# Performance work log

Hardware: AMD Instinct MI355X
Metric: run time of the kernel (lower is better)

## Reference

```python
import jax, jax.numpy as jnp
import numpy as np

PI = float(np.pi)
C64 = jnp.complex64

# ---- gate matrices (PennyLane conventions) ----

def _rx(t):
    c = jnp.cos(t / 2); s = jnp.sin(t / 2)
    return jnp.array([[c, -1j * s], [-1j * s, c]]).astype(C64)

def _rz(t):
    return jnp.array([[jnp.exp(-0.5j * t), 0.0], [0.0, jnp.exp(0.5j * t)]]).astype(C64)

def _rot(phi, th, om):
    # Rot(phi, theta, omega) = RZ(omega) RY(theta) RZ(phi)
    c = jnp.cos(th / 2); s = jnp.sin(th / 2)
    return jnp.array([
        [jnp.exp(-0.5j * (phi + om)) * c, -jnp.exp(0.5j * (phi - om)) * s],
        [jnp.exp(-0.5j * (phi - om)) * s,  jnp.exp(0.5j * (phi + om)) * c],
    ]).astype(C64)

def _crx(t):
    c = jnp.cos(t / 2); s = jnp.sin(t / 2)
    return jnp.array([
        [1, 0, 0, 0],
        [0, 1, 0, 0],
        [0, 0, c, -1j * s],
        [0, 0, -1j * s, c],
    ]).astype(C64)

CNOT = jnp.array([[1, 0, 0, 0], [0, 1, 0, 0], [0, 0, 0, 1], [0, 0, 1, 0]], dtype=C64)

# ---- state-vector primitives (state shape (2,)*n) ----

def _ap1(psi, U, w):
    return jnp.moveaxis(jnp.tensordot(U, psi, axes=((1,), (w,))), 0, w)

def _ap2(psi, U, a, b):
    U = U.reshape(2, 2, 2, 2)
    return jnp.moveaxis(jnp.tensordot(U, psi, axes=((2, 3), (a, b))), (0, 1), (a, b))

def _expZ(psi, w):
    p = jnp.moveaxis(jnp.abs(psi) ** 2, w, 0)
    return (p[0] - p[1]).sum()

def _expX(psi, w):
    return jnp.real(jnp.sum(jnp.conj(psi) * jnp.flip(psi, axis=w)))

# wire pairs in initQKV_on_wires order
_PAIRS = [(0, 1), (1, 2), (2, 3), (3, 0), (0, 3), (1, 0), (2, 1), (3, 2)]

def _init_qkv(psi, rot_p, crx_p, off):
    for i, (a, b) in enumerate(_PAIRS):
        psi = _ap1(psi, _rot(rot_p[3 * i], rot_p[3 * i + 1], rot_p[3 * i + 2]), off + a)
        psi = _ap2(psi, _crx(crx_p[i]), off + a, off + b)
        psi = _ap2(psi, CNOT, off + a, off + b)
    return psi

def _sample(x, qr, qc, kr, kc, vr, vc):
    # qmha_score: 8-qubit circuit
    psi = jnp.zeros((2,) * 8, C64).at[(0,) * 8].set(1.0)
    for w in range(4):  # AngleEmbedding (RX) of xq
        psi = _ap1(psi, _rx(x[w]), w)
    psi = _init_qkv(psi, qr, qc, 0)
    for w in range(4):  # AngleEmbedding (RX) of xk (same x)
        psi = _ap1(psi, _rx(x[w]), w)
    psi = _init_qkv(psi, kr, kc, 4)
    for w in range(4):
        psi = _ap2(psi, CNOT, w, w + 4)
    z = jnp.stack([_expZ(psi, w) for w in range(4)])
    xm = jnp.stack([_expX(psi, w) for w in range(4)])
    score = jnp.sqrt(z * z + xm * xm)
    # qmha_value: 4-qubit circuit
    phi = jnp.zeros((2,) * 4, C64).at[(0,) * 4].set(1.0)
    for w in range(4):
        phi = _ap1(phi, _rx(x[w]), w)
    phi = _init_qkv(phi, vr, vc, 0)
    for w in range(4):
        phi = _ap1(phi, _rz(jnp.tanh(score[w]) * PI), w)
    for a, b in [(0, 1), (1, 2), (2, 3)]:
        phi = _ap2(phi, CNOT, a, b)
    zv = jnp.stack([_expZ(phi, w) for w in range(4)])
    xv = jnp.stack([_expX(phi, w) for w in range(4)])
    return jnp.concatenate([zv, xv])  # [8]


def setup_inputs() -> dict:
    key = jax.random.key(0)
    ks = jax.random.split(key, 12)
    B = 16384
    u = lambda k, n: jax.random.uniform(k, (n,), jnp.float32, -PI / 2, PI / 2)
    return {
        "x1": jax.random.normal(ks[0], (B, 96), jnp.float32),
        "pre_w": jax.random.normal(ks[1], (4, 96), jnp.float32) / np.sqrt(96.0),
        "pre_b": jnp.zeros((4,), jnp.float32),
        "q_rot": u(ks[2], 24),
        "k_rot": u(ks[3], 24),
        "v_rot": u(ks[4], 24),
        "q_crx": 0.1 * jax.random.normal(ks[5], (8,), jnp.float32),
        "k_crx": 0.1 * jax.random.normal(ks[6], (8,), jnp.float32),
        "v_crx": 0.1 * jax.random.normal(ks[7], (8,), jnp.float32),
        "ln_w": jnp.ones((8,), jnp.float32),
        "ln_b": jnp.zeros((8,), jnp.float32),
        "head_w": jax.random.normal(ks[8], (2, 8), jnp.float32) / np.sqrt(8.0),
        "head_b": jnp.zeros((2,), jnp.float32),
    }


def reference(x1, pre_w, pre_b, q_rot, k_rot, v_rot, q_crx, k_crx, v_crx,
              ln_w, ln_b, head_w, head_b):
    x = x1 @ pre_w.T + pre_b  # [B, 4] angles
    outs = jax.vmap(lambda xi: _sample(xi, q_rot, q_crx, k_rot, k_crx, v_rot, v_crx))(x)  # [B, 8]
    mu = outs.mean(-1, keepdims=True)
    var = outs.var(-1, keepdims=True)
    y = (outs - mu) / jnp.sqrt(var + 1e-5) * ln_w + ln_b  # LayerNorm(8)
    g = jax.nn.gelu(y, approximate=False)  # torch nn.GELU default = exact erf
    return g @ head_w.T + head_b  # [B, 2]
```

## Files before the change

kernel.cpp:

```cpp
#include <hip/hip_runtime.h>
#include <math.h>

#define PI_F 3.14159265358979323846f

struct c32 { float x, y; };

__device__ __forceinline__ c32 cmul(c32 a, c32 b){ return { a.x*b.x - a.y*b.y, a.x*b.y + a.y*b.x }; }
__device__ __forceinline__ c32 cadd(c32 a, c32 b){ return { a.x+b.x, a.y+b.y }; }

__device__ __forceinline__ void apply_1q(c32 s[16], const int w, c32 A, c32 B, c32 C, c32 D){
  const int m = 8 >> w;
  #pragma unroll
  for (int i = 0; i < 16; i++){
    if (i & m) continue;
    c32 a = s[i], b = s[i | m];
    s[i]     = cadd(cmul(A,a), cmul(B,b));
    s[i | m] = cadd(cmul(C,a), cmul(D,b));
  }
}

__device__ __forceinline__ void apply_rx(c32 s[16], const int w, float c, float sn){
  const int m = 8 >> w;
  #pragma unroll
  for (int i = 0; i < 16; i++){
    if (i & m) continue;
    c32 a = s[i], b = s[i | m];
    s[i]     = { c*a.x + sn*b.y, c*a.y - sn*b.x };
    s[i | m] = { c*b.x + sn*a.y, c*b.y - sn*a.x };
  }
}

__device__ __forceinline__ void apply_crx(c32 s[16], const int wa, const int wb, float c, float sn){
  const int ma = 8 >> wa, mb = 8 >> wb;
  #pragma unroll
  for (int i = 0; i < 16; i++){
    if (!(i & ma) || (i & mb)) continue;
    c32 a = s[i], b = s[i | mb];
    s[i]      = { c*a.x + sn*b.y, c*a.y - sn*b.x };
    s[i | mb] = { c*b.x + sn*a.y, c*b.y - sn*a.x };
  }
}

__device__ __forceinline__ void apply_cnot(c32 s[16], const int wa, const int wb){
  const int ma = 8 >> wa, mb = 8 >> wb;
  #pragma unroll
  for (int i = 0; i < 16; i++){
    if (!(i & ma) || (i & mb)) continue;
    c32 t = s[i]; s[i] = s[i | mb]; s[i | mb] = t;
  }
}

__device__ __forceinline__ void apply_rz(c32 s[16], const int w, float c, float sn){
  const int m = 8 >> w;
  #pragma unroll
  for (int i = 0; i < 16; i++){
    c32 a = s[i];
    float sg = (i & m) ? sn : -sn;
    s[i] = { c*a.x - sg*a.y, c*a.y + sg*a.x };
  }
}

__device__ __forceinline__ void init_qkv(c32 s[16],
                                         const float* __restrict__ rotp,
                                         const float* __restrict__ crxp){
  constexpr int pa[8] = {0,1,2,3,0,1,2,3};
  constexpr int pb[8] = {1,2,3,0,3,0,1,2};
  #pragma unroll
  for (int g = 0; g < 8; g++){
    float phi = rotp[3*g], th = rotp[3*g+1], om = rotp[3*g+2];
    float c, sn, ca, sa, cb, sb;
    __sincosf(0.5f*th,       &sn, &c);
    __sincosf(0.5f*(phi+om), &sa, &ca);
    __sincosf(0.5f*(phi-om), &sb, &cb);
    c32 A{  c*ca, -c*sa }, Bm{ -sn*cb, -sn*sb }, C{ sn*cb, -sn*sb }, D{ c*ca, c*sa };
    apply_1q(s, pa[g], A, Bm, C, D);
    float cc, cs; __sincosf(0.5f*crxp[g], &cs, &cc);
    apply_crx(s, pa[g], pb[g], cc, cs);
    apply_cnot(s, pa[g], pb[g]);
  }
}

__device__ __forceinline__ float expZ(const c32 s[16], const int w){
  const int m = 8 >> w;
  float r = 0.f;
  #pragma unroll
  for (int i = 0; i < 16; i++){
    float p = s[i].x*s[i].x + s[i].y*s[i].y;
    r += (i & m) ? -p : p;
  }
  return r;
}

__device__ __forceinline__ float expX(const c32 s[16], const int w){
  const int m = 8 >> w;
  float r = 0.f;
  #pragma unroll
  for (int i = 0; i < 16; i++){
    if (i & m) continue;
    r += s[i].x*s[(i|m)].x + s[i].y*s[(i|m)].y;
  }
  return 2.f*r;
}

#define LDS_STRIDE 97

__global__ __launch_bounds__(64, 1) void qc_main(
    const float* __restrict__ x1,
    const float* __restrict__ pre_w, const float* __restrict__ pre_b,
    const float* __restrict__ q_rot, const float* __restrict__ k_rot, const float* __restrict__ v_rot,
    const float* __restrict__ q_crx, const float* __restrict__ k_crx, const float* __restrict__ v_crx,
    const float* __restrict__ ln_w, const float* __restrict__ ln_b,
    const float* __restrict__ head_w, const float* __restrict__ head_b,
    float* __restrict__ out, int B){

  __shared__ float xs[64 * LDS_STRIDE];
  const int t = threadIdx.x;
  const int base = blockIdx.x * 64;

  {
    int rem = B - base; if (rem > 64) rem = 64;
    const int nf4 = rem * 24;
    const float4* src = (const float4*)(x1 + (long)base * 96);
    #pragma unroll
    for (int k = 0; k < 24; k++){
      int g = t + 64*k;
      if (g < nf4){
        float4 v = src[g];
        int f = 4*g;
        int r = f / 96, cidx = f - 96*r;
        float* d = &xs[r*LDS_STRIDE + cidx];
        d[0]=v.x; d[1]=v.y; d[2]=v.z; d[3]=v.w;
      }
    }
  }
  __syncthreads();

  float xw[4];
  {
    float a0 = pre_b[0], a1 = pre_b[1], a2 = pre_b[2], a3 = pre_b[3];
    const float* row = &xs[t * LDS_STRIDE];
    #pragma unroll
    for (int j = 0; j < 96; j++){
      float v = row[j];
      a0 += v * pre_w[j];
      a1 += v * pre_w[96  + j];
      a2 += v * pre_w[192 + j];
      a3 += v * pre_w[288 + j];
    }
    xw[0]=a0; xw[1]=a1; xw[2]=a2; xw[3]=a3;
  }

  float cw[4], sw[4];
  #pragma unroll
  for (int w = 0; w < 4; w++) __sincosf(0.5f*xw[w], &sw[w], &cw[w]);

  float cxk[4];
  {
    c32 ks[16];
    #pragma unroll
    for (int i = 0; i < 16; i++) ks[i] = {0.f, 0.f};
    ks[0] = {1.f, 0.f};
    init_qkv(ks, k_rot, k_crx);
    #pragma unroll
    for (int w = 0; w < 4; w++) cxk[w] = expX(ks, w);
  }

  c32 rx16[16];
  #pragma unroll
  for (int i = 0; i < 16; i++) rx16[i] = {0.f, 0.f};
  rx16[0] = {1.f, 0.f};
  #pragma unroll
  for (int w = 0; w < 4; w++) apply_rx(rx16, w, cw[w], sw[w]);

  float thc[4], ths[4];
  {
    c32 st[16];
    #pragma unroll
    for (int i = 0; i < 16; i++) st[i] = rx16[i];
    init_qkv(st, q_rot, q_crx);
    #pragma unroll
    for (int w = 0; w < 4; w++) apply_rx(st, w, cw[w], sw[w]);
    #pragma unroll
    for (int w = 0; w < 4; w++){
      float z  = expZ(st, w);
      float xm = expX(st, w) * cxk[w];
      float score = sqrtf(z*z + xm*xm);
      float th = tanhf(score) * PI_F;
      __sincosf(0.5f*th, &ths[w], &thc[w]);
    }
  }

  float o[8];
  {
    c32 st[16];
    #pragma unroll
    for (int i = 0; i < 16; i++) st[i] = rx16[i];
    init_qkv(st, v_rot, v_crx);
    #pragma unroll
    for (int w = 0; w < 4; w++) apply_rz(st, w, thc[w], ths[w]);
    apply_cnot(st, 0, 1);
    apply_cnot(st, 1, 2);
    apply_cnot(st, 2, 3);
    #pragma unroll
    for (int w = 0; w < 4; w++){ o[w] = expZ(st, w); o[4+w] = expX(st, w); }
  }

  float mu = 0.f;
  #pragma unroll
  for (int j = 0; j < 8; j++) mu += o[j];
  mu *= 0.125f;
  float var = 0.f;
  #pragma unroll
  for (int j = 0; j < 8; j++){ float d = o[j] - mu; var += d*d; }
  var *= 0.125f;
  float inv = rsqrtf(var + 1e-5f);
  float h0 = head_b[0], h1 = head_b[1];
  #pragma unroll
  for (int j = 0; j < 8; j++){
    float y = (o[j] - mu) * inv * ln_w[j] + ln_b[j];
    float g = 0.5f * y * (1.f + erff(y * 0.70710678118f));
    h0 += g * head_w[j];
    h1 += g * head_w[8 + j];
  }

  const int sid = base + t;
  if (sid < B){
    float2 r2; r2.x = h0; r2.y = h1;
    ((float2*)out)[sid] = r2;
  }
}

extern "C" void kernel_launch(void* const* d_in, const int* in_sizes, int n_in,
                              void* d_out, int out_size, void* d_ws, size_t ws_size,
                              hipStream_t stream) {
  const float* x1     = (const float*)d_in[0];
  const float* pre_w  = (const float*)d_in[1];
  const float* pre_b  = (const float*)d_in[2];
  const float* q_rot  = (const float*)d_in[3];
  const float* k_rot  = (const float*)d_in[4];
  const float* v_rot  = (const float*)d_in[5];
  const float* q_crx  = (const float*)d_in[6];
  const float* k_crx  = (const float*)d_in[7];
  const float* v_crx  = (const float*)d_in[8];
  const float* ln_w   = (const float*)d_in[9];
  const float* ln_b   = (const float*)d_in[10];
  const float* head_w = (const float*)d_in[11];
  const float* head_b = (const float*)d_in[12];
  float* out = (float*)d_out;
  (void)d_ws; (void)ws_size; (void)n_in; (void)out_size;

  const int B = in_sizes[0] / 96;
  const int nb = (B + 63) / 64;
  qc_main<<<nb, 64, 0, stream>>>(x1, pre_w, pre_b,
                                 q_rot, k_rot, v_rot,
                                 q_crx, k_crx, v_crx,
                                 ln_w, ln_b, head_w, head_b,
                                 out, B);
}
```

Baseline: 102.6 us.

## Precompute gate coefficients in setup kernel and algebraically simplify circuit simulation

Adds a one-block setup kernel that computes the Rot/CRX coefficients and the key-circuit expX values once and writes them to workspace, so the main kernel no longer evaluates per-thread trig for every gate. The main kernel builds the RX product state in closed form, fuses CRX with CNOT, folds the final RX layer and the RZ+CNOT chain into modified Z/X measurements and diagonal phases, and swaps tanhf for an exp-based tanh. Exact erf GELU is replaced by the tanh approximation, which adds small numeric error. The extra launch adds fixed overhead.

```diff
diff --git a/kernel.cpp b/kernel.cpp
--- a/kernel.cpp
+++ b/kernel.cpp
@@ -5,101 +5,108 @@
 
 struct c32 { float x, y; };
 
-__device__ __forceinline__ c32 cmul(c32 a, c32 b){ return { a.x*b.x - a.y*b.y, a.x*b.y + a.y*b.x }; }
-__device__ __forceinline__ c32 cadd(c32 a, c32 b){ return { a.x+b.x, a.y+b.y }; }
-
-__device__ __forceinline__ void apply_1q(c32 s[16], const int w, c32 A, c32 B, c32 C, c32 D){
+
+__device__ __forceinline__ void apply_rot_red(c32* s, const int w,
+                                              float Ax, float Ay, float Cx, float Cy){
   const int m = 8 >> w;
   #pragma unroll
   for (int i = 0; i < 16; i++){
     if (i & m) continue;
     c32 a = s[i], b = s[i | m];
-    s[i]     = cadd(cmul(A,a), cmul(B,b));
-    s[i | m] = cadd(cmul(C,a), cmul(D,b));
-  }
-}
-
-__device__ __forceinline__ void apply_rx(c32 s[16], const int w, float c, float sn){
-  const int m = 8 >> w;
-  #pragma unroll
-  for (int i = 0; i < 16; i++){
-    if (i & m) continue;
-    c32 a = s[i], b = s[i | m];
-    s[i]     = { c*a.x + sn*b.y, c*a.y - sn*b.x };
-    s[i | m] = { c*b.x + sn*a.y, c*b.y - sn*a.x };
-  }
-}
-
-__device__ __forceinline__ void apply_crx(c32 s[16], const int wa, const int wb, float c, float sn){
+    s[i].x     = Ax*a.x - Ay*a.y - Cx*b.x - Cy*b.y;
+    s[i].y     = Ax*a.y + Ay*a.x - Cx*b.y + Cy*b.x;
+    s[i | m].x = Cx*a.x - Cy*a.y + Ax*b.x + Ay*b.y;
+    s[i | m].y = Cx*a.y + Cy*a.x + Ax*b.y - Ay*b.x;
+  }
+}
+
+__device__ __forceinline__ void apply_crxnot(c32* s, const int wa, const int wb,
+                                             float c, float sn){
   const int ma = 8 >> wa, mb = 8 >> wb;
   #pragma unroll
   for (int i = 0; i < 16; i++){
     if (!(i & ma) || (i & mb)) continue;
-    c32 a = s[i], b = s[i | mb];
-    s[i]      = { c*a.x + sn*b.y, c*a.y - sn*b.x };
-    s[i | mb] = { c*b.x + sn*a.y, c*b.y - sn*a.x };
-  }
-}
-
-__device__ __forceinline__ void apply_cnot(c32 s[16], const int wa, const int wb){
-  const int ma = 8 >> wa, mb = 8 >> wb;
-  #pragma unroll
-  for (int i = 0; i < 16; i++){
-    if (!(i & ma) || (i & mb)) continue;
-    c32 t = s[i]; s[i] = s[i | mb]; s[i | mb] = t;
-  }
-}
-
-__device__ __forceinline__ void apply_rz(c32 s[16], const int w, float c, float sn){
-  const int m = 8 >> w;
-  #pragma unroll
-  for (int i = 0; i < 16; i++){
-    c32 a = s[i];
-    float sg = (i & m) ? sn : -sn;
-    s[i] = { c*a.x - sg*a.y, c*a.y + sg*a.x };
-  }
-}
-
-__device__ __forceinline__ void init_qkv(c32 s[16],
-                                         const float* __restrict__ rotp,
-                                         const float* __restrict__ crxp){
+    c32 u = s[i], v = s[i | mb];
+    s[i]      = { c*v.x + sn*u.y, c*v.y - sn*u.x };
+    s[i | mb] = { c*u.x + sn*v.y, c*u.y - sn*v.x };
+  }
+}
+
+__device__ __forceinline__ void sim_initqkv(c32* s, const float* __restrict__ gp){
   constexpr int pa[8] = {0,1,2,3,0,1,2,3};
   constexpr int pb[8] = {1,2,3,0,3,0,1,2};
   #pragma unroll
   for (int g = 0; g < 8; g++){
+    const float* q = gp + 8*g;
+    apply_rot_red(s, pa[g], q[0], q[1], q[2], q[3]);
+    apply_crxnot(s, pa[g], pb[g], q[4], q[5]);
+  }
+}
+
+__device__ __forceinline__ void build_rx(c32* s, const float* cw, const float* sw){
+  float m01[4] = { cw[0]*cw[1], cw[0]*sw[1], sw[0]*cw[1], sw[0]*sw[1] };
+  float m23[4] = { cw[2]*cw[3], cw[2]*sw[3], sw[2]*cw[3], sw[2]*sw[3] };
+  #pragma unroll
+  for (int i = 0; i < 16; i++){
+    float mag = m01[(i >> 2) & 3] * m23[i & 3];
+    const int pc = __popc(i) & 3;
+    s[i] = (pc == 0) ? c32{ mag, 0.f } :
+           (pc == 1) ? c32{ 0.f, -mag } :
+           (pc == 2) ? c32{ -mag, 0.f } : c32{ 0.f, mag };
+  }
+}
+
+__device__ __forceinline__ float fast_tanh(float x){
+  float e = __expf(2.f * x);
+  return 1.f - 2.f * __builtin_amdgcn_rcpf(e + 1.f);
+}
+
+__global__ __launch_bounds__(64) void qc_setup(
+    const float* __restrict__ q_rot, const float* __restrict__ k_rot, const float* __restrict__ v_rot,
+    const float* __restrict__ q_crx, const float* __restrict__ k_crx, const float* __restrict__ v_crx,
+    float* __restrict__ ws){
+  __shared__ float kg[64];
+  const int t = threadIdx.x;
+  if (t < 24){
+    const int grp = t >> 3, g = t & 7;
+    const float* rotp = grp == 0 ? q_rot : (grp == 1 ? k_rot : v_rot);
+    const float* crxp = grp == 0 ? q_crx : (grp == 1 ? k_crx : v_crx);
     float phi = rotp[3*g], th = rotp[3*g+1], om = rotp[3*g+2];
-    float c, sn, ca, sa, cb, sb;
-    __sincosf(0.5f*th,       &sn, &c);
+    float c, s, ca, sa, cb, sb;
+    __sincosf(0.5f*th,       &s,  &c);
     __sincosf(0.5f*(phi+om), &sa, &ca);
     __sincosf(0.5f*(phi-om), &sb, &cb);
-    c32 A{  c*ca, -c*sa }, Bm{ -sn*cb, -sn*sb }, C{ sn*cb, -sn*sb }, D{ c*ca, c*sa };
-    apply_1q(s, pa[g], A, Bm, C, D);
     float cc, cs; __sincosf(0.5f*crxp[g], &cs, &cc);
-    apply_crx(s, pa[g], pb[g], cc, cs);
-    apply_cnot(s, pa[g], pb[g]);
-  }
-}
-
-__device__ __forceinline__ float expZ(const c32 s[16], const int w){
-  const int m = 8 >> w;
-  float r = 0.f;
-  #pragma unroll
-  for (int i = 0; i < 16; i++){
-    float p = s[i].x*s[i].x + s[i].y*s[i].y;
-    r += (i & m) ? -p : p;
-  }
-  return r;
-}
-
-__device__ __forceinline__ float expX(const c32 s[16], const int w){
-  const int m = 8 >> w;
-  float r = 0.f;
-  #pragma unroll
-  for (int i = 0; i < 16; i++){
-    if (i & m) continue;
-    r += s[i].x*s[(i|m)].x + s[i].y*s[(i|m)].y;
-  }
-  return 2.f*r;
+    float vals[6] = { c*ca, -c*sa, s*cb, -s*sb, cc, cs };
+    if (grp == 1){
+      #pragma unroll
+      for (int j = 0; j < 6; j++) kg[8*g + j] = vals[j];
+    } else {
+      float* dst = ws + (grp == 0 ? 0 : 64) + 8*g;
+      #pragma unroll
+      for (int j = 0; j < 6; j++) dst[j] = vals[j];
+      dst[6] = 0.f; dst[7] = 0.f;
+    }
+  }
+  __syncthreads();
+  c32 st[16];
+  #pragma unroll
+  for (int i = 0; i < 16; i++) st[i] = { 0.f, 0.f };
+  st[0] = { 1.f, 0.f };
+  sim_initqkv(st, kg);
+  if (t == 0){
+    #pragma unroll
+    for (int w = 0; w < 4; w++){
+      const int m = 8 >> w;
+      float r = 0.f;
+      #pragma unroll
+      for (int i = 0; i < 16; i++){
+        if (i & m) continue;
+        r += st[i].x*st[i|m].x + st[i].y*st[i|m].y;
+      }
+      ws[128 + w] = 2.f * r;
+    }
+  }
 }
 
 #define LDS_STRIDE 97
@@ -107,10 +114,9 @@
 __global__ __launch_bounds__(64, 1) void qc_main(
     const float* __restrict__ x1,
     const float* __restrict__ pre_w, const float* __restrict__ pre_b,
-    const float* __restrict__ q_rot, const float* __restrict__ k_rot, const float* __restrict__ v_rot,
-    const float* __restrict__ q_crx, const float* __restrict__ k_crx, const float* __restrict__ v_crx,
     const float* __restrict__ ln_w, const float* __restrict__ ln_b,
     const float* __restrict__ head_w, const float* __restrict__ head_b,
+    const float* __restrict__ ws,
     float* __restrict__ out, int B){
 
   __shared__ float xs[64 * LDS_STRIDE];
@@ -154,55 +160,82 @@
   #pragma unroll
   for (int w = 0; w < 4; w++) __sincosf(0.5f*xw[w], &sw[w], &cw[w]);
 
-  float cxk[4];
-  {
-    c32 ks[16];
-    #pragma unroll
-    for (int i = 0; i < 16; i++) ks[i] = {0.f, 0.f};
-    ks[0] = {1.f, 0.f};
-    init_qkv(ks, k_rot, k_crx);
-    #pragma unroll
-    for (int w = 0; w < 4; w++) cxk[w] = expX(ks, w);
-  }
-
-  c32 rx16[16];
-  #pragma unroll
-  for (int i = 0; i < 16; i++) rx16[i] = {0.f, 0.f};
-  rx16[0] = {1.f, 0.f};
-  #pragma unroll
-  for (int w = 0; w < 4; w++) apply_rx(rx16, w, cw[w], sw[w]);
-
-  float thc[4], ths[4];
-  {
-    c32 st[16];
-    #pragma unroll
-    for (int i = 0; i < 16; i++) st[i] = rx16[i];
-    init_qkv(st, q_rot, q_crx);
-    #pragma unroll
-    for (int w = 0; w < 4; w++) apply_rx(st, w, cw[w], sw[w]);
-    #pragma unroll
-    for (int w = 0; w < 4; w++){
-      float z  = expZ(st, w);
-      float xm = expX(st, w) * cxk[w];
+  c32 st[16];
+
+  float cr[4], sr[4];
+  {
+    build_rx(st, cw, sw);
+    sim_initqkv(st, ws);
+    float p[16];
+    #pragma unroll
+    for (int i = 0; i < 16; i++) p[i] = st[i].x*st[i].x + st[i].y*st[i].y;
+    #pragma unroll
+    for (int w = 0; w < 4; w++){
+      const int m = 8 >> w;
+      float sz = 0.f, sx = 0.f, sy = 0.f;
+      #pragma unroll
+      for (int i = 0; i < 16; i++) sz += (i & m) ? -p[i] : p[i];
+      #pragma unroll
+      for (int i = 0; i < 16; i++){
+        if (i & m) continue;
+        c32 a = st[i], b = st[i|m];
+        sx += a.x*b.x + a.y*b.y;
+        sy += a.x*b.y - a.y*b.x;
+      }
+      float cth = 1.f - 2.f*sw[w]*sw[w];
+      float sth = 2.f*sw[w]*cw[w];
+      float z   = cth*sz + sth*(2.f*sy);
+      float xm  = (2.f*sx) * ws[128 + w];
       float score = sqrtf(z*z + xm*xm);
-      float th = tanhf(score) * PI_F;
-      __sincosf(0.5f*th, &ths[w], &thc[w]);
+      float th = fast_tanh(score) * PI_F;
+      __sincosf(0.5f*th, &sr[w], &cr[w]);
     }
   }
 
   float o[8];
   {
-    c32 st[16];
-    #pragma unroll
-    for (int i = 0; i < 16; i++) st[i] = rx16[i];
-    init_qkv(st, v_rot, v_crx);
-    #pragma unroll
-    for (int w = 0; w < 4; w++) apply_rz(st, w, thc[w], ths[w]);
-    apply_cnot(st, 0, 1);
-    apply_cnot(st, 1, 2);
-    apply_cnot(st, 2, 3);
-    #pragma unroll
-    for (int w = 0; w < 4; w++){ o[w] = expZ(st, w); o[4+w] = expX(st, w); }
+    build_rx(st, cw, sw);
+    sim_initqkv(st, ws + 64);
+    float p[16];
+    #pragma unroll
+    for (int i = 0; i < 16; i++) p[i] = st[i].x*st[i].x + st[i].y*st[i].y;
+    constexpr int zm[4] = {8, 12, 14, 15};
+    #pragma unroll
+    for (int w = 0; w < 4; w++){
+      float r = 0.f;
+      #pragma unroll
+      for (int i = 0; i < 16; i++)
+        r += (__popc(i & zm[w]) & 1) ? -p[i] : p[i];
+      o[w] = r;
+    }
+    c32 ph01[4], ph23[4];
+    ph01[0] = { cr[0]*cr[1] - sr[0]*sr[1], -(cr[0]*sr[1] + sr[0]*cr[1]) };
+    ph01[1] = { cr[0]*cr[1] + sr[0]*sr[1],   cr[0]*sr[1] - sr[0]*cr[1] };
+    ph01[2] = { ph01[1].x, -ph01[1].y };
+    ph01[3] = { ph01[0].x, -ph01[0].y };
+    ph23[0] = { cr[2]*cr[3] - sr[2]*sr[3], -(cr[2]*sr[3] + sr[2]*cr[3]) };
+    ph23[1] = { cr[2]*cr[3] + sr[2]*sr[3],   cr[2]*sr[3] - sr[2]*cr[3] };
+    ph23[2] = { ph23[1].x, -ph23[1].y };
+    ph23[3] = { ph23[0].x, -ph23[0].y };
+    #pragma unroll
+    for (int i = 0; i < 16; i++){
+      c32 a = st[i], f = ph01[(i >> 2) & 3], g2 = ph23[i & 3];
+      c32 b = { a.x*f.x - a.y*f.y, a.x*f.y + a.y*f.x };
+      st[i] = { b.x*g2.x - b.y*g2.y, b.x*g2.y + b.y*g2.x };
+    }
+    constexpr int xmk[4] = {12, 6, 3, 1};
+    constexpr int hb[4]  = {8, 4, 2, 1};
+    #pragma unroll
+    for (int w = 0; w < 4; w++){
+      float r = 0.f;
+      #pragma unroll
+      for (int i = 0; i < 16; i++){
+        if (i & hb[w]) continue;
+        const int j = i ^ xmk[w];
+        r += st[i].x*st[j].x + st[i].y*st[j].y;
+      }
+      o[4 + w] = 2.f * r;
+    }
   }
 
   float mu = 0.f;
@@ -218,7 +251,8 @@
   #pragma unroll
   for (int j = 0; j < 8; j++){
     float y = (o[j] - mu) * inv * ln_w[j] + ln_b[j];
-    float g = 0.5f * y * (1.f + erff(y * 0.70710678118f));
+    float u = 0.7978845608f * (y + 0.044715f*y*y*y);
+    float g = 0.5f * y * (1.f + fast_tanh(u));
     h0 += g * head_w[j];
     h1 += g * head_w[8 + j];
   }
@@ -247,13 +281,13 @@
   const float* head_w = (const float*)d_in[11];
   const float* head_b = (const float*)d_in[12];
   float* out = (float*)d_out;
-  (void)d_ws; (void)ws_size; (void)n_in; (void)out_size;
+  float* ws  = (float*)d_ws;
+  (void)ws_size; (void)n_in; (void)out_size;
+
+  qc_setup<<<1, 64, 0, stream>>>(q_rot, k_rot, v_rot, q_crx, k_crx, v_crx, ws);
 
   const int B = in_sizes[0] / 96;
   const int nb = (B + 63) / 64;
-  qc_main<<<nb, 64, 0, stream>>>(x1, pre_w, pre_b,
-                                 q_rot, k_rot, v_rot,
-                                 q_crx, k_crx, v_crx,
-                                 ln_w, ln_b, head_w, head_b,
-                                 out, B);
-}
+  qc_main<<<nb, 64, 0, stream>>>(x1, pre_w, pre_b, ln_w, ln_b, head_w, head_b,
+                                 (const float*)ws, out, B);
+}
```

Measured after the change: 106.1 us. 1.03x slower.
